# Performance work log

Hardware: AMD Instinct MI355X
Metric: run time of the kernel (lower is better)

The kernel has to match this reference:

```python
import jax, jax.numpy as jnp
import numpy as np
from jax import lax

SLOPE = 0.01  # nn.LeakyReLU default negative slope

def leaky(x):
    return jnp.where(x >= 0, x, SLOPE * x)

def conv2d(x, w, b, pad):
    # x: [N,C,H,W], w: [O,I,kh,kw]
    y = lax.conv_general_dilated(x, w, (1, 1), [(pad, pad), (pad, pad)],
                                 dimension_numbers=('NCHW', 'OIHW', 'NCHW'))
    return y + b[None, :, None, None]

def centered_ifftn(x, axes):
    # np.fft.fftshift(np.fft.ifftn(np.fft.ifftshift(X), norm='ortho'))
    return jnp.fft.fftshift(jnp.fft.ifftn(jnp.fft.ifftshift(x, axes=axes), axes=axes, norm='ortho'), axes=axes)

def setup_inputs() -> dict:
    key = jax.random.key(0)
    ks = jax.random.split(key, 10)
    B, H, W, CK = 8, 640, 368, 32
    return {
        'img':    jax.random.normal(ks[0], (B, 1, H, W), jnp.float32),
        'kspace': jax.random.normal(ks[1], (B, 2, H, W), jnp.float32),
        # k_model1: Conv2d(2, CK, 3, padding=1) + LeakyReLU
        'wk': jax.random.normal(ks[2], (CK, 2, 3, 3), jnp.float32) * 0.1,
        'bk': jnp.zeros((CK,), jnp.float32),
        # conv1: Conv2d(CK, 2, kernel_size=1)
        'w1': jax.random.normal(ks[3], (2, CK, 1, 1), jnp.float32) * 0.1,
        'b1': jnp.zeros((2,), jnp.float32),
        # conv2: Conv2d(2, 1, kernel_size=1)
        'w2': jax.random.normal(ks[4], (1, 2, 1, 1), jnp.float32) * 0.1,
        'b2': jnp.zeros((1,), jnp.float32),
        # i_model1: Conv2d(1, 1, 3, padding=1) + LeakyReLU
        'wi': jax.random.normal(ks[5], (1, 1, 3, 3), jnp.float32) * 0.1,
        'bi': jnp.zeros((1,), jnp.float32),
    }

def reference(img, kspace, wk, bk, w1, b1, w2, b2, wi, bi):
    # k-space branch: k_model1 then conv1 + LeakyReLU
    out1 = leaky(conv2d(leaky(conv2d(kspace, wk, bk, 1)), w1, b1, 0))  # [B,2,H,W]
    # channel 0 = real, channel 1 = imag; ifftn over ALL axes (incl. batch),
    # exactly as the original numpy call with axes=range(out.ndim)
    cplx = out1[:, 0].astype(jnp.complex64) + 1j * out1[:, 1].astype(jnp.complex64)  # [B,H,W]
    im = jnp.abs(centered_ifftn(cplx, (0, 1, 2)))[:, None]  # [B,1,H,W]
    # concat with image, cast to half (torch.cuda.HalfTensor), conv2 + LeakyReLU
    out = jnp.concatenate([im, img], axis=1).astype(jnp.float16)  # [B,2,H,W]
    out = leaky(conv2d(out, w2.astype(jnp.float16), b2.astype(jnp.float16), 0))
    out = out.astype(jnp.float32)  # [B,1,H,W]
    # image-domain model
    return leaky(conv2d(out, wi, bi, 1))  # [B,1,H,W]
```

## Files before the change

### kernel.cpp

```cpp
#include <hip/hip_runtime.h>
#include <hip/hip_fp16.h>
#include <math.h>

#define B_ 8
#define H_ 640
#define W_ 368
#define HW_ (H_*W_)
#define NP_ (B_*H_*W_)

#define WLINES 8
#define HCOLS 4
#define TS 16

typedef __attribute__((ext_vector_type(8))) short v8s;
typedef __attribute__((ext_vector_type(4))) float v4f;

__device__ __forceinline__ float leaky_(float x){ return x >= 0.f ? x : 0.01f*x; }

__device__ __forceinline__ unsigned short f2bf(float x){
    unsigned u = __float_as_uint(x);
    u += 0x7FFFu + ((u >> 16) & 1u);
    return (unsigned short)(u >> 16);
}

__device__ __forceinline__ float2 cadd_(float2 a, float2 b){ return make_float2(a.x+b.x, a.y+b.y); }
__device__ __forceinline__ float2 csub_(float2 a, float2 b){ return make_float2(a.x-b.x, a.y-b.y); }
__device__ __forceinline__ float2 cmul_(float2 a, float c, float s){
    return make_float2(a.x*c - a.y*s, a.x*s + a.y*c);
}
__device__ __forceinline__ float2 cmulv_(float2 a, float2 w){
    return make_float2(a.x*w.x - a.y*w.y, a.x*w.y + a.y*w.x);
}

__device__ __forceinline__ void dft4p_(float2 p0, float2 p1, float2 p2, float2 p3,
                                       float2& z0, float2& z1, float2& z2, float2& z3){
    float2 s0 = cadd_(p0,p2), d0 = csub_(p0,p2);
    float2 s1 = cadd_(p1,p3), d1 = csub_(p1,p3);
    z0 = cadd_(s0,s1);
    z2 = csub_(s0,s1);
    z1 = make_float2(d0.x - d1.y, d0.y + d1.x);
    z3 = make_float2(d0.x + d1.y, d0.y - d1.x);
}

__device__ __forceinline__ void fft16p_(const float2* x, float2* X){
    const float C1 = 0.9238795325112867f, S1 = 0.3826834323650898f;
    const float R  = 0.7071067811865476f;
    float2 Y[4][4];
    #pragma unroll
    for (int b = 0; b < 4; ++b)
        dft4p_(x[b], x[4+b], x[8+b], x[12+b], Y[b][0], Y[b][1], Y[b][2], Y[b][3]);
    Y[1][1] = cmul_(Y[1][1],  C1,  S1);
    Y[1][2] = cmul_(Y[1][2],   R,   R);
    Y[1][3] = cmul_(Y[1][3],  S1,  C1);
    Y[2][1] = cmul_(Y[2][1],   R,   R);
    Y[2][2] = make_float2(-Y[2][2].y, Y[2][2].x);
    Y[2][3] = cmul_(Y[2][3],  -R,   R);
    Y[3][1] = cmul_(Y[3][1],  S1,  C1);
    Y[3][2] = cmul_(Y[3][2],  -R,   R);
    Y[3][3] = cmul_(Y[3][3], -C1, -S1);
    #pragma unroll
    for (int c = 0; c < 4; ++c)
        dft4p_(Y[0][c], Y[1][c], Y[2][c], Y[3][c], X[c], X[c+4], X[c+8], X[c+12]);
}

__device__ __forceinline__ void fft8p_(const float2* x, float2* X){
    const float R = 0.7071067811865476f;
    float2 Y0[4], Y1[4];
    dft4p_(x[0], x[2], x[4], x[6], Y0[0], Y0[1], Y0[2], Y0[3]);
    dft4p_(x[1], x[3], x[5], x[7], Y1[0], Y1[1], Y1[2], Y1[3]);
    float2 T0 = Y1[0];
    float2 T1 = cmul_(Y1[1],  R, R);
    float2 T2 = make_float2(-Y1[2].y, Y1[2].x);
    float2 T3 = cmul_(Y1[3], -R, R);
    X[0] = cadd_(Y0[0], T0);  X[4] = csub_(Y0[0], T0);
    X[1] = cadd_(Y0[1], T1);  X[5] = csub_(Y0[1], T1);
    X[2] = cadd_(Y0[2], T2);  X[6] = csub_(Y0[2], T2);
    X[3] = cadd_(Y0[3], T3);  X[7] = csub_(Y0[3], T3);
}

__global__ void init_tables_kernel(float2* __restrict__ T){
    int i = blockIdx.x*blockDim.x + threadIdx.x;
    if (i >= 1301) return;
    int r, c, modN; int j;
    if      (i <  368){ j = i;        r = j%16; c = j/16; modN = 368; }
    else if (i < 1008){ j = i-368;    r = j%16; c = j/16; modN = 640; }
    else if (i < 1048){ j = i-1008;   r = j%8;  c = j/8;  modN = 40;  }
    else              { j = i-1048;   r = j/11; c = j%11 + 1; modN = 23; }
    int t = (int)(((long long)r * c) % modN);
    if (t > modN/2) t -= modN;
    float ang = (float)(6.283185307179586 * ((double)t / (double)modN));
    float s, co;
    sincosf(ang, &s, &co);
    T[i] = make_float2(co, s);
}

__global__ __launch_bounds__(256) void kbranch_mfma(const float* __restrict__ ksp,
                               const float* __restrict__ wk,
                               const float* __restrict__ bk,
                               const float* __restrict__ w1,
                               const float* __restrict__ b1,
                               float2* __restrict__ A){
    __shared__ unsigned short Sb[2616];
    __shared__ unsigned short Wr[4*512];
    int t = threadIdx.x;
    int bh = blockIdx.x;
    int h = bh % 640, b = bh / 640;

    for (int i = t; i < 2616; i += 256){
        float val = 0.f;
        if (i < 2232){
            int rr = i / 372, col = i - rr*372;
            int r = rr >> 1, ic = rr & 1;
            int hh = h - 1 + r, sc = col - 1;
            if ((unsigned)hh < 640u && (unsigned)sc < 368u)
                val = ksp[((b*2 + ic)*640 + hh)*368 + sc];
        }
        Sb[i] = f2bf(val);
    }

    int lane = t & 63, wave = t >> 6;
    int oc = lane & 15, q = lane >> 4;
    int off[8];
    v8s bf0, bf1, b2f;
    #pragma unroll
    for (int j = 0; j < 8; ++j){
        int kk = q*8 + j;
        if (kk < 18){
            int ic = (kk >= 9) ? 1 : 0;
            int tt = kk - ic*9;
            int ty = tt/3, tx = tt - ty*3;
            off[j] = (ty*2 + ic)*372 + tx;
            bf0[j] = (short)f2bf(wk[oc*18 + kk]);
            bf1[j] = (short)f2bf(wk[(oc+16)*18 + kk]);
        } else {
            off[j] = 2232;
            bf0[j] = 0; bf1[j] = 0;
        }
        b2f[j] = (oc < 2) ? (short)f2bf(w1[oc*32 + kk]) : (short)0;
    }
    float bk0 = bk[oc], bk1 = bk[oc+16];
    float biasn = (oc == 1) ? b1[1] : b1[0];
    unsigned short* Wrw = Wr + (wave << 9);
    __syncthreads();

    int gbase = wave*6;
    int cnt = (wave < 3) ? 6 : 5;
    for (int i = 0; i < cnt; ++i){
        int g = gbase + i;
        int w0m = g*16 + oc;
        v8s af;
        #pragma unroll
        for (int j = 0; j < 8; ++j) af[j] = (short)Sb[off[j] + w0m];
        v4f d0 = {0.f,0.f,0.f,0.f}, d1 = {0.f,0.f,0.f,0.f};
        d0 = __builtin_amdgcn_mfma_f32_16x16x32_bf16(af, bf0, d0, 0, 0, 0);
        d1 = __builtin_amdgcn_mfma_f32_16x16x32_bf16(af, bf1, d1, 0, 0, 0);
        #pragma unroll
        for (int r = 0; r < 4; ++r){
            int px = q*4 + r;
            Wrw[px*32 + oc]      = f2bf(leaky_(d0[r] + bk0));
            Wrw[px*32 + 16 + oc] = f2bf(leaky_(d1[r] + bk1));
        }
        asm volatile("s_waitcnt lgkmcnt(0)" ::: "memory");
        const v8s* ap = (const v8s*)(Wrw + oc*32);
        v8s a2 = ap[q];
        v4f d2 = {0.f,0.f,0.f,0.f};
        d2 = __builtin_amdgcn_mfma_f32_16x16x32_bf16(a2, b2f, d2, 0, 0, 0);
        float vals[4], ov[4];
        #pragma unroll
        for (int r = 0; r < 4; ++r){
            vals[r] = leaky_(biasn + d2[r]);
            ov[r] = __shfl_xor(vals[r], 1);
        }
        if (oc == 0){
            float2* dst = A + (size_t)bh*368 + g*16 + q*4;
            *(float4*)dst       = make_float4(vals[0], ov[0], vals[1], ov[1]);
            *(float4*)(dst + 2) = make_float4(vals[2], ov[2], vals[3], ov[3]);
        }
        asm volatile("s_waitcnt lgkmcnt(0)" ::: "memory");
    }
}

__global__ __launch_bounds__(256) void fftW_kernel(const float2* __restrict__ A,
                                                   const float2* __restrict__ TW368P,
                                                   const float2* __restrict__ F23P,
                                                   float2* __restrict__ Bo){
    __shared__ float2 X[WLINES*369];
    int t = threadIdx.x;
    size_t base = (size_t)blockIdx.x * (WLINES*368);

    for (int i = t; i < WLINES*368; i += 256){
        int l = i / 368, n = i - l*368;
        float2 v = A[base + i];
        float s = (i & 1) ? -1.f : 1.f;
        X[l*369 + n] = make_float2(v.x*s, v.y*s);
    }
    __syncthreads();

    if (t < 184){
        int l = t & 7, n2 = t >> 3;
        float2 xr[16], Xo[16];
        #pragma unroll
        for (int n1 = 0; n1 < 16; ++n1) xr[n1] = X[l*369 + 23*n1 + n2];
        fft16p_(xr, Xo);
        const float2* row = TW368P + n2*16;
        #pragma unroll
        for (int k1 = 0; k1 < 16; ++k1)
            X[l*369 + 23*k1 + n2] = cmulv_(Xo[k1], row[k1]);
    }
    __syncthreads();

    {
        int l = t & 7, k1 = (t >> 3) & 15, half = t >> 7;
        const float2* xp = X + l*369 + 23*k1;
        float2 x0 = xp[0];
        float2 u[11], d[11];
        #pragma unroll
        for (int m = 1; m <= 11; ++m){
            float2 a = xp[m], bb = xp[23-m];
            u[m-1] = cadd_(a, bb);
            d[m-1] = csub_(a, bb);
        }
        __syncthreads();
        int k2beg = half ? 12 : 0;
        int k2end = half ? 23 : 12;
        for (int k2 = k2beg; k2 < k2end; ++k2){
            const float2* row = F23P + k2*11;
            float re = x0.x, im = x0.y;
            #pragma unroll
            for (int m = 0; m < 11; ++m){
                float c = row[m].x, s = row[m].y;
                re += u[m].x*c - d[m].y*s;
                im += u[m].y*c + d[m].x*s;
            }
            X[l*369 + k1 + 16*k2] = make_float2(re, im);
        }
    }
    __syncthreads();

    const float sc = 0.052129458158616354f;
    for (int i = t; i < WLINES*368; i += 256){
        int l = i / 368, k = i - l*368;
        float2 v = X[l*369 + k];
        float s = (i & 1) ? -sc : sc;
        Bo[base + i] = make_float2(v.x*s, v.y*s);
    }
}

__global__ __launch_bounds__(256) void fftH_kernel(const float2* __restrict__ Bi,
                                                   const float2* __restrict__ TW640P,
                                                   const float2* __restrict__ TW40P,
                                                   float2* __restrict__ Ao){
    __shared__ float2 X[640*5];
    int t = threadIdx.x;
    int b  = blockIdx.x / 92;
    int w0 = (blockIdx.x - b*92) * HCOLS;
    const float2* src = Bi + (size_t)b*HW_ + w0;

    for (int i = t; i < 640*HCOLS; i += 256){
        int n = i >> 2, c = i & 3;
        float2 v = src[(size_t)n*W_ + c];
        float s = (n & 1) ? -1.f : 1.f;
        X[n*5 + c] = make_float2(v.x*s, v.y*s);
    }
    __syncthreads();

    if (t < 160){
        int c = t & 3, n2 = t >> 2;
        float2 xr[16], Xo[16];
        #pragma unroll
        for (int n1 = 0; n1 < 16; ++n1) xr[n1] = X[(40*n1 + n2)*5 + c];
        fft16p_(xr, Xo);
        const float2* row = TW640P + n2*16;
        #pragma unroll
        for (int k1 = 0; k1 < 16; ++k1)
            X[(40*k1 + n2)*5 + c] = cmulv_(Xo[k1], row[k1]);
    }
    __syncthreads();

    for (int it = t; it < 320; it += 256){
        int c = it & 3, k1 = (it >> 2) & 15, m2 = it >> 6;
        float2 xr[8], Xo[8];
        #pragma unroll
        for (int m1 = 0; m1 < 8; ++m1) xr[m1] = X[(40*k1 + 5*m1 + m2)*5 + c];
        fft8p_(xr, Xo);
        const float2* row = TW40P + m2*8;
        #pragma unroll
        for (int j1 = 0; j1 < 8; ++j1)
            X[(40*k1 + 5*j1 + m2)*5 + c] = cmulv_(Xo[j1], row[j1]);
    }
    __syncthreads();

    {
        const float CK1[5] = {1.f,  0.30901699437494745f, -0.8090169943749475f, -0.8090169943749475f,  0.30901699437494745f};
        const float SK1[5] = {0.f,  0.9510565162951535f,   0.5877852522924731f, -0.5877852522924731f, -0.9510565162951535f};
        const float CK2[5] = {1.f, -0.8090169943749475f,   0.30901699437494745f, 0.30901699437494745f, -0.8090169943749475f};
        const float SK2[5] = {0.f,  0.5877852522924731f,  -0.9510565162951535f,  0.9510565162951535f, -0.5877852522924731f};
        int it0 = t, it1 = t + 256;
        int c0 = it0 & 3, k10 = (it0 >> 2) & 15, j10 = it0 >> 6;
        int c1 = it1 & 3, k11 = (it1 >> 2) & 15, j11 = it1 >> 6;
        float2 p0[5], p1[5];
        #pragma unroll
        for (int m2 = 0; m2 < 5; ++m2) p0[m2] = X[(40*k10 + 5*j10 + m2)*5 + c0];
        #pragma unroll
        for (int m2 = 0; m2 < 5; ++m2) p1[m2] = X[(40*k11 + 5*j11 + m2)*5 + c1];
        __syncthreads();
        float2 u0a = cadd_(p0[1], p0[4]), d0a = csub_(p0[1], p0[4]);
        float2 u0b = cadd_(p0[2], p0[3]), d0b = csub_(p0[2], p0[3]);
        float2 u1a = cadd_(p1[1], p1[4]), d1a = csub_(p1[1], p1[4]);
        float2 u1b = cadd_(p1[2], p1[3]), d1b = csub_(p1[2], p1[3]);
        #pragma unroll
        for (int j2 = 0; j2 < 5; ++j2){
            float c1v = CK1[j2], s1v = SK1[j2], c2v = CK2[j2], s2v = SK2[j2];
            float re0 = p0[0].x + u0a.x*c1v - d0a.y*s1v + u0b.x*c2v - d0b.y*s2v;
            float im0 = p0[0].y + u0a.y*c1v + d0a.x*s1v + u0b.y*c2v + d0b.x*s2v;
            float re1 = p1[0].x + u1a.x*c1v - d1a.y*s1v + u1b.x*c2v - d1b.y*s2v;
            float im1 = p1[0].y + u1a.y*c1v + d1a.x*s1v + u1b.y*c2v + d1b.x*s2v;
            X[(k10 + 16*j10 + 128*j2)*5 + c0] = make_float2(re0, im0);
            X[(k11 + 16*j11 + 128*j2)*5 + c1] = make_float2(re1, im1);
        }
    }
    __syncthreads();

    const float sc = 0.03952847075210474f;
    float2* dst = Ao + (size_t)b*HW_ + w0;
    for (int i = t; i < 640*HCOLS; i += 256){
        int k = i >> 2, c = i & 3;
        float2 v = X[k*5 + c];
        float s = (k & 1) ? -sc : sc;
        dst[(size_t)k*W_ + c] = make_float2(v.x*s, v.y*s);
    }
}

__global__ __launch_bounds__(256) void tail_kernel(const float2* __restrict__ A,
                                  const float* __restrict__ img,
                                  const float* __restrict__ w2,
                                  const float* __restrict__ b2,
                                  const float* __restrict__ wi,
                                  const float* __restrict__ bi,
                                  float* __restrict__ out){
    __shared__ float Pl[8][TS+2][TS+2];
    int t = threadIdx.x;
    int ty0 = (blockIdx.x / 23) * TS;
    int tx0 = (blockIdx.x % 23) * TS;

    float w2h0 = __half2float(__float2half(w2[0]));
    float w2h1 = __half2float(__float2half(w2[1]));
    float b2h  = __half2float(__float2half(b2[0]));
    const float sc8 = 0.35355339059327373f;

    for (int idx = t; idx < (TS+2)*(TS+2); idx += 256){
        int hy = idx / (TS+2), hx = idx - hy*(TS+2);
        int hh = ty0 - 1 + hy, ww = tx0 - 1 + hx;
        bool inb = (hh >= 0) && (hh < H_) && (ww >= 0) && (ww < W_);
        int hc = min(max(hh, 0), H_-1), wc = min(max(ww, 0), W_-1);
        int hw = hc*W_ + wc;
        float2 x[8], Xo[8];
        #pragma unroll
        for (int n = 0; n < 8; ++n){
            float2 v = A[(size_t)n*HW_ + hw];
            float s = (n & 1) ? -1.f : 1.f;
            x[n] = make_float2(v.x*s, v.y*s);
        }
        fft8p_(x, Xo);
        float inbf = inb ? 1.f : 0.f;
        #pragma unroll
        for (int k = 0; k < 8; ++k){
            float s = (k & 1) ? -sc8 : sc8;
            float yr = Xo[k].x * s, yi = Xo[k].y * s;
            float mag = sqrtf(yr*yr + yi*yi);
            float a = __half2float(__float2half(mag));
            float g = __half2float(__float2half(img[(size_t)k*HW_ + hw]));
            float o = a*w2h0 + g*w2h1 + b2h;
            o = leaky_(o);
            o = __half2float(__float2half(o));
            Pl[k][hy][hx] = o * inbf;
        }
    }
    __syncthreads();

    int sy = t >> 4, sx = t & 15;
    float wv[9];
    #pragma unroll
    for (int q = 0; q < 9; ++q) wv[q] = wi[q];
    float bi0 = bi[0];
    #pragma unroll
    for (int k = 0; k < 8; ++k){
        float acc = bi0;
        #pragma unroll
        for (int dy = 0; dy < 3; ++dy)
            #pragma unroll
            for (int dx = 0; dx < 3; ++dx)
                acc += wv[dy*3+dx] * Pl[k][sy+dy][sx+dx];
        out[((size_t)k*H_ + ty0+sy)*W_ + tx0+sx] = leaky_(acc);
    }
}

extern "C" void kernel_launch(void* const* d_in, const int* in_sizes, int n_in,
                              void* d_out, int out_size, void* d_ws, size_t ws_size,
                              hipStream_t stream){
    const float* img = (const float*)d_in[0];
    const float* ksp = (const float*)d_in[1];
    const float* wk  = (const float*)d_in[2];
    const float* bk  = (const float*)d_in[3];
    const float* w1  = (const float*)d_in[4];
    const float* b1  = (const float*)d_in[5];
    const float* w2  = (const float*)d_in[6];
    const float* b2  = (const float*)d_in[7];
    const float* wi  = (const float*)d_in[8];
    const float* bi  = (const float*)d_in[9];

    char* ws = (char*)d_ws;
    float2* A   = (float2*)(ws + 0);
    float2* Bb  = (float2*)(ws + 15073280);
    float2* T   = (float2*)(ws + 30146560);
    float2* TW368P = T + 0;
    float2* TW640P = T + 368;
    float2* TW40P  = T + 1008;
    float2* F23P   = T + 1048;
    float* out  = (float*)d_out;

    init_tables_kernel<<<6, 256, 0, stream>>>(T);

    kbranch_mfma<<<B_*H_, 256, 0, stream>>>(ksp, wk, bk, w1, b1, A);

    fftW_kernel<<<(B_*H_)/WLINES, 256, 0, stream>>>(A, TW368P, F23P, Bb);
    fftH_kernel<<<B_*(W_/HCOLS), 256, 0, stream>>>(Bb, TW640P, TW40P, A);

    tail_kernel<<<(H_/TS)*(W_/TS), 256, 0, stream>>>(A, img, w2, b2, wi, bi, out);
}
```

Measured before the change: 172.6 us.

## Stage im2col patches in LDS for vectorized MFMA A-fragment loads

The k-branch conv kernel now builds a per-row im2col matrix in shared memory (368 pixels × 40 padded taps) instead of a raw halo tile. Each MFMA A-fragment becomes one 16-byte LDS load rather than eight scattered 2-byte loads. The intermediate 32-channel activations are written back into the same buffer as packed pairs, with the w1 weight order permuted to match, and one waitcnt and the separate Wr buffer are dropped. Leaky ReLU becomes fmaxf. The risks are a slower staging phase (strided stores, 144 active threads issuing scalar global loads) and possible races from reusing M across waves.

New measurement: 173.5 us. Within noise of the previous version (+0.5%).

```diff
diff --git a/kernel.cpp b/kernel.cpp
--- a/kernel.cpp
+++ b/kernel.cpp
@@ -15,7 +15,7 @@
 typedef __attribute__((ext_vector_type(8))) short v8s;
 typedef __attribute__((ext_vector_type(4))) float v4f;
 
-__device__ __forceinline__ float leaky_(float x){ return x >= 0.f ? x : 0.01f*x; }
+__device__ __forceinline__ float leaky_(float x){ return fmaxf(x, 0.01f*x); }
 
 __device__ __forceinline__ unsigned short f2bf(float x){
     unsigned u = __float_as_uint(x);
@@ -100,69 +100,69 @@
                                const float* __restrict__ w1,
                                const float* __restrict__ b1,
                                float2* __restrict__ A){
-    __shared__ unsigned short Sb[2616];
-    __shared__ unsigned short Wr[4*512];
+    __shared__ unsigned short M[368*40];
     int t = threadIdx.x;
     int bh = blockIdx.x;
     int h = bh % 640, b = bh / 640;
-
-    for (int i = t; i < 2616; i += 256){
-        float val = 0.f;
-        if (i < 2232){
-            int rr = i / 372, col = i - rr*372;
-            int r = rr >> 1, ic = rr & 1;
-            int hh = h - 1 + r, sc = col - 1;
-            if ((unsigned)hh < 640u && (unsigned)sc < 368u)
-                val = ksp[((b*2 + ic)*640 + hh)*368 + sc];
-        }
-        Sb[i] = f2bf(val);
-    }
-
     int lane = t & 63, wave = t >> 6;
-    int oc = lane & 15, q = lane >> 4;
-    int off[8];
+    int n = lane & 15, q = lane >> 4;
+
     v8s bf0, bf1, b2f;
     #pragma unroll
     for (int j = 0; j < 8; ++j){
         int kk = q*8 + j;
-        if (kk < 18){
-            int ic = (kk >= 9) ? 1 : 0;
-            int tt = kk - ic*9;
-            int ty = tt/3, tx = tt - ty*3;
-            off[j] = (ty*2 + ic)*372 + tx;
-            bf0[j] = (short)f2bf(wk[oc*18 + kk]);
-            bf1[j] = (short)f2bf(wk[(oc+16)*18 + kk]);
-        } else {
-            off[j] = 2232;
-            bf0[j] = 0; bf1[j] = 0;
-        }
-        b2f[j] = (oc < 2) ? (short)f2bf(w1[oc*32 + kk]) : (short)0;
-    }
-    float bk0 = bk[oc], bk1 = bk[oc+16];
-    float biasn = (oc == 1) ? b1[1] : b1[0];
-    unsigned short* Wrw = Wr + (wave << 9);
+        float v0 = (kk < 18) ? wk[n*18 + kk]      : 0.f;
+        float v1 = (kk < 18) ? wk[(n+16)*18 + kk] : 0.f;
+        bf0[j] = (short)f2bf(v0);
+        bf1[j] = (short)f2bf(v1);
+        int ko = (kk & 1) ? 16 + (kk >> 1) : (kk >> 1);
+        b2f[j] = (n < 2) ? (short)f2bf(w1[n*32 + ko]) : (short)0;
+    }
+    float bk0 = bk[n], bk1 = bk[n+16];
+    float biasn = (n == 1) ? b1[1] : b1[0];
+
+    if (t < 144){
+        int kk = t >> 3, px0 = t & 7;
+        int ic = (kk >= 9) ? 1 : 0;
+        int tt = kk - 9*ic;
+        int ty = tt / 3, tx = tt - 3*ty;
+        int hh = h - 1 + ty;
+        float rvf = ((unsigned)hh < 640u) ? 1.f : 0.f;
+        int hhc = min(max(hh, 0), 639);
+        const float* base = ksp + ((size_t)(b*2 + ic)*640 + hhc)*368;
+        int txo = tx - 1;
+        for (int px = px0; px < 368; px += 8){
+            int c = px + txo;
+            float msk = ((unsigned)c < 368u) ? rvf : 0.f;
+            int cc = min(max(c, 0), 367);
+            M[px*40 + kk] = f2bf(base[cc] * msk);
+        }
+    } else {
+        int kk = 18 + ((t - 144) >> 3), px0 = (t - 144) & 7;
+        for (int px = px0; px < 368; px += 8)
+            M[px*40 + kk] = 0;
+    }
     __syncthreads();
 
     int gbase = wave*6;
     int cnt = (wave < 3) ? 6 : 5;
     for (int i = 0; i < cnt; ++i){
         int g = gbase + i;
-        int w0m = g*16 + oc;
-        v8s af;
-        #pragma unroll
-        for (int j = 0; j < 8; ++j) af[j] = (short)Sb[off[j] + w0m];
+        int pxa = g*16 + n;
+        const v8s af = *(const v8s*)(M + pxa*40 + q*8);
         v4f d0 = {0.f,0.f,0.f,0.f}, d1 = {0.f,0.f,0.f,0.f};
         d0 = __builtin_amdgcn_mfma_f32_16x16x32_bf16(af, bf0, d0, 0, 0, 0);
         d1 = __builtin_amdgcn_mfma_f32_16x16x32_bf16(af, bf1, d1, 0, 0, 0);
         #pragma unroll
         for (int r = 0; r < 4; ++r){
-            int px = q*4 + r;
-            Wrw[px*32 + oc]      = f2bf(leaky_(d0[r] + bk0));
-            Wrw[px*32 + 16 + oc] = f2bf(leaky_(d1[r] + bk1));
+            int px = g*16 + q*4 + r;
+            float l0 = leaky_(d0[r] + bk0);
+            float l1 = leaky_(d1[r] + bk1);
+            unsigned pk = ((unsigned)f2bf(l1) << 16) | (unsigned)f2bf(l0);
+            *(unsigned*)(M + px*40 + 2*n) = pk;
         }
         asm volatile("s_waitcnt lgkmcnt(0)" ::: "memory");
-        const v8s* ap = (const v8s*)(Wrw + oc*32);
-        v8s a2 = ap[q];
+        const v8s a2 = *(const v8s*)(M + pxa*40 + q*8);
         v4f d2 = {0.f,0.f,0.f,0.f};
         d2 = __builtin_amdgcn_mfma_f32_16x16x32_bf16(a2, b2f, d2, 0, 0, 0);
         float vals[4], ov[4];
@@ -171,12 +171,11 @@
             vals[r] = leaky_(biasn + d2[r]);
             ov[r] = __shfl_xor(vals[r], 1);
         }
-        if (oc == 0){
+        if (n == 0){
             float2* dst = A + (size_t)bh*368 + g*16 + q*4;
             *(float4*)dst       = make_float4(vals[0], ov[0], vals[1], ov[1]);
             *(float4*)(dst + 2) = make_float4(vals[2], ov[2], vals[3], ov[3]);
         }
-        asm volatile("s_waitcnt lgkmcnt(0)" ::: "memory");
     }
 }
 
```

## Transpose intermediate after W-FFT so H-FFT reads contiguous columns

Applied to the files above, without the earlier changes.

The W-direction FFT now writes its output transposed ([b][w][h]), so the H-direction FFT kernel loads contiguous 640-element lines instead of strided 4-column gathers. It uses a padded per-line shared layout in place of the interleaved one. The tail kernel now reads the transposed layout and iterates its halo with h as the fast index to keep reads coalesced, which splits its work into two LDS passes. The change trades coalescing on the W-FFT store (8 consecutive h values per k) for contiguous H-FFT loads and stores, and it also makes leaky_ branchless via fmaxf.

Result: no change. 172.8 us (+0.1%).

```diff
diff --git a/kernel.cpp b/kernel.cpp
--- a/kernel.cpp
+++ b/kernel.cpp
@@ -9,13 +9,14 @@
 #define NP_ (B_*H_*W_)
 
 #define WLINES 8
-#define HCOLS 4
+#define HLINES 4
+#define HP 645
 #define TS 16
 
 typedef __attribute__((ext_vector_type(8))) short v8s;
 typedef __attribute__((ext_vector_type(4))) float v4f;
 
-__device__ __forceinline__ float leaky_(float x){ return x >= 0.f ? x : 0.01f*x; }
+__device__ __forceinline__ float leaky_(float x){ return fmaxf(x, 0.01f*x); }
 
 __device__ __forceinline__ unsigned short f2bf(float x){
     unsigned u = __float_as_uint(x);
@@ -183,7 +184,7 @@
 __global__ __launch_bounds__(256) void fftW_kernel(const float2* __restrict__ A,
                                                    const float2* __restrict__ TW368P,
                                                    const float2* __restrict__ F23P,
-                                                   float2* __restrict__ Bo){
+                                                   float2* __restrict__ Bt){
     __shared__ float2 X[WLINES*369];
     int t = threadIdx.x;
     size_t base = (size_t)blockIdx.x * (WLINES*368);
@@ -191,7 +192,7 @@
     for (int i = t; i < WLINES*368; i += 256){
         int l = i / 368, n = i - l*368;
         float2 v = A[base + i];
-        float s = (i & 1) ? -1.f : 1.f;
+        float s = (n & 1) ? -1.f : 1.f;
         X[l*369 + n] = make_float2(v.x*s, v.y*s);
     }
     __syncthreads();
@@ -238,55 +239,55 @@
     __syncthreads();
 
     const float sc = 0.052129458158616354f;
+    int b  = blockIdx.x / 80;
+    int h0 = (blockIdx.x - b*80) * WLINES;
     for (int i = t; i < WLINES*368; i += 256){
-        int l = i / 368, k = i - l*368;
+        int k = i >> 3, l = i & 7;
         float2 v = X[l*369 + k];
-        float s = (i & 1) ? -sc : sc;
-        Bo[base + i] = make_float2(v.x*s, v.y*s);
-    }
-}
-
-__global__ __launch_bounds__(256) void fftH_kernel(const float2* __restrict__ Bi,
+        float s = (k & 1) ? -sc : sc;
+        Bt[((size_t)(b*368 + k))*640 + h0 + l] = make_float2(v.x*s, v.y*s);
+    }
+}
+
+__global__ __launch_bounds__(256) void fftH_kernel(const float2* __restrict__ Bt,
                                                    const float2* __restrict__ TW640P,
                                                    const float2* __restrict__ TW40P,
-                                                   float2* __restrict__ Ao){
-    __shared__ float2 X[640*5];
+                                                   float2* __restrict__ A2){
+    __shared__ float2 X[HLINES*HP];
     int t = threadIdx.x;
-    int b  = blockIdx.x / 92;
-    int w0 = (blockIdx.x - b*92) * HCOLS;
-    const float2* src = Bi + (size_t)b*HW_ + w0;
-
-    for (int i = t; i < 640*HCOLS; i += 256){
-        int n = i >> 2, c = i & 3;
-        float2 v = src[(size_t)n*W_ + c];
+    size_t base = (size_t)blockIdx.x * (HLINES*640);
+
+    for (int i = t; i < HLINES*640; i += 256){
+        int l = i / 640, n = i - l*640;
+        float2 v = Bt[base + i];
         float s = (n & 1) ? -1.f : 1.f;
-        X[n*5 + c] = make_float2(v.x*s, v.y*s);
+        X[l*HP + n] = make_float2(v.x*s, v.y*s);
     }
     __syncthreads();
 
     if (t < 160){
-        int c = t & 3, n2 = t >> 2;
+        int l = t & 3, n2 = t >> 2;
         float2 xr[16], Xo[16];
         #pragma unroll
-        for (int n1 = 0; n1 < 16; ++n1) xr[n1] = X[(40*n1 + n2)*5 + c];
+        for (int n1 = 0; n1 < 16; ++n1) xr[n1] = X[l*HP + 40*n1 + n2];
         fft16p_(xr, Xo);
         const float2* row = TW640P + n2*16;
         #pragma unroll
         for (int k1 = 0; k1 < 16; ++k1)
-            X[(40*k1 + n2)*5 + c] = cmulv_(Xo[k1], row[k1]);
+            X[l*HP + 40*k1 + n2] = cmulv_(Xo[k1], row[k1]);
     }
     __syncthreads();
 
     for (int it = t; it < 320; it += 256){
-        int c = it & 3, k1 = (it >> 2) & 15, m2 = it >> 6;
+        int l = it & 3, k1 = (it >> 2) & 15, m2 = it >> 6;
         float2 xr[8], Xo[8];
         #pragma unroll
-        for (int m1 = 0; m1 < 8; ++m1) xr[m1] = X[(40*k1 + 5*m1 + m2)*5 + c];
+        for (int m1 = 0; m1 < 8; ++m1) xr[m1] = X[l*HP + 40*k1 + 5*m1 + m2];
         fft8p_(xr, Xo);
         const float2* row = TW40P + m2*8;
         #pragma unroll
         for (int j1 = 0; j1 < 8; ++j1)
-            X[(40*k1 + 5*j1 + m2)*5 + c] = cmulv_(Xo[j1], row[j1]);
+            X[l*HP + 40*k1 + 5*j1 + m2] = cmulv_(Xo[j1], row[j1]);
     }
     __syncthreads();
 
@@ -296,13 +297,13 @@
         const float CK2[5] = {1.f, -0.8090169943749475f,   0.30901699437494745f, 0.30901699437494745f, -0.8090169943749475f};
         const float SK2[5] = {0.f,  0.5877852522924731f,  -0.9510565162951535f,  0.9510565162951535f, -0.5877852522924731f};
         int it0 = t, it1 = t + 256;
-        int c0 = it0 & 3, k10 = (it0 >> 2) & 15, j10 = it0 >> 6;
-        int c1 = it1 & 3, k11 = (it1 >> 2) & 15, j11 = it1 >> 6;
+        int l0 = it0 & 3, k10 = (it0 >> 2) & 15, j10 = it0 >> 6;
+        int l1 = it1 & 3, k11 = (it1 >> 2) & 15, j11 = it1 >> 6;
         float2 p0[5], p1[5];
         #pragma unroll
-        for (int m2 = 0; m2 < 5; ++m2) p0[m2] = X[(40*k10 + 5*j10 + m2)*5 + c0];
-        #pragma unroll
-        for (int m2 = 0; m2 < 5; ++m2) p1[m2] = X[(40*k11 + 5*j11 + m2)*5 + c1];
+        for (int m2 = 0; m2 < 5; ++m2) p0[m2] = X[l0*HP + 40*k10 + 5*j10 + m2];
+        #pragma unroll
+        for (int m2 = 0; m2 < 5; ++m2) p1[m2] = X[l1*HP + 40*k11 + 5*j11 + m2];
         __syncthreads();
         float2 u0a = cadd_(p0[1], p0[4]), d0a = csub_(p0[1], p0[4]);
         float2 u0b = cadd_(p0[2], p0[3]), d0b = csub_(p0[2], p0[3]);
@@ -315,30 +316,29 @@
             float im0 = p0[0].y + u0a.y*c1v + d0a.x*s1v + u0b.y*c2v + d0b.x*s2v;
             float re1 = p1[0].x + u1a.x*c1v - d1a.y*s1v + u1b.x*c2v - d1b.y*s2v;
             float im1 = p1[0].y + u1a.y*c1v + d1a.x*s1v + u1b.y*c2v + d1b.x*s2v;
-            X[(k10 + 16*j10 + 128*j2)*5 + c0] = make_float2(re0, im0);
-            X[(k11 + 16*j11 + 128*j2)*5 + c1] = make_float2(re1, im1);
+            X[l0*HP + k10 + 16*j10 + 128*j2] = make_float2(re0, im0);
+            X[l1*HP + k11 + 16*j11 + 128*j2] = make_float2(re1, im1);
         }
     }
     __syncthreads();
 
     const float sc = 0.03952847075210474f;
-    float2* dst = Ao + (size_t)b*HW_ + w0;
-    for (int i = t; i < 640*HCOLS; i += 256){
-        int k = i >> 2, c = i & 3;
-        float2 v = X[k*5 + c];
+    for (int i = t; i < HLINES*640; i += 256){
+        int l = i / 640, k = i - l*640;
+        float2 v = X[l*HP + k];
         float s = (k & 1) ? -sc : sc;
-        dst[(size_t)k*W_ + c] = make_float2(v.x*s, v.y*s);
-    }
-}
-
-__global__ __launch_bounds__(256) void tail_kernel(const float2* __restrict__ A,
+        A2[base + i] = make_float2(v.x*s, v.y*s);
+    }
+}
+
+__global__ __launch_bounds__(256) void tail_kernel(const float2* __restrict__ A2,
                                   const float* __restrict__ img,
                                   const float* __restrict__ w2,
                                   const float* __restrict__ b2,
                                   const float* __restrict__ wi,
                                   const float* __restrict__ bi,
                                   float* __restrict__ out){
-    __shared__ float Pl[8][TS+2][TS+2];
+    __shared__ float Pl[8][TS+2][TS+3];
     int t = threadIdx.x;
     int ty0 = (blockIdx.x / 23) * TS;
     int tx0 = (blockIdx.x % 23) * TS;
@@ -347,31 +347,40 @@
     float w2h1 = __half2float(__float2half(w2[1]));
     float b2h  = __half2float(__float2half(b2[0]));
     const float sc8 = 0.35355339059327373f;
+
+    for (int idx = t; idx < (TS+2)*(TS+2); idx += 256){
+        int hx = idx / (TS+2), hy = idx - hx*(TS+2);
+        int hh = ty0 - 1 + hy, ww = tx0 - 1 + hx;
+        int hc = min(max(hh, 0), H_-1), wc = min(max(ww, 0), W_-1);
+        float2 x[8], Xo[8];
+        #pragma unroll
+        for (int n = 0; n < 8; ++n){
+            float2 v = A2[((size_t)(n*368 + wc))*640 + hc];
+            float s = (n & 1) ? -1.f : 1.f;
+            x[n] = make_float2(v.x*s, v.y*s);
+        }
+        fft8p_(x, Xo);
+        #pragma unroll
+        for (int k = 0; k < 8; ++k){
+            float s = (k & 1) ? -sc8 : sc8;
+            float yr = Xo[k].x * s, yi = Xo[k].y * s;
+            float mag = sqrtf(yr*yr + yi*yi);
+            Pl[k][hy][hx] = __half2float(__float2half(mag));
+        }
+    }
+    __syncthreads();
 
     for (int idx = t; idx < (TS+2)*(TS+2); idx += 256){
         int hy = idx / (TS+2), hx = idx - hy*(TS+2);
         int hh = ty0 - 1 + hy, ww = tx0 - 1 + hx;
         bool inb = (hh >= 0) && (hh < H_) && (ww >= 0) && (ww < W_);
         int hc = min(max(hh, 0), H_-1), wc = min(max(ww, 0), W_-1);
-        int hw = hc*W_ + wc;
-        float2 x[8], Xo[8];
-        #pragma unroll
-        for (int n = 0; n < 8; ++n){
-            float2 v = A[(size_t)n*HW_ + hw];
-            float s = (n & 1) ? -1.f : 1.f;
-            x[n] = make_float2(v.x*s, v.y*s);
-        }
-        fft8p_(x, Xo);
         float inbf = inb ? 1.f : 0.f;
         #pragma unroll
         for (int k = 0; k < 8; ++k){
-            float s = (k & 1) ? -sc8 : sc8;
-            float yr = Xo[k].x * s, yi = Xo[k].y * s;
-            float mag = sqrtf(yr*yr + yi*yi);
-            float a = __half2float(__float2half(mag));
-            float g = __half2float(__float2half(img[(size_t)k*HW_ + hw]));
-            float o = a*w2h0 + g*w2h1 + b2h;
-            o = leaky_(o);
+            float g = __half2float(__float2half(img[(size_t)k*HW_ + hc*W_ + wc]));
+            float a = Pl[k][hy][hx];
+            float o = leaky_(a*w2h0 + g*w2h1 + b2h);
             o = __half2float(__float2half(o));
             Pl[k][hy][hx] = o * inbf;
         }
@@ -411,7 +420,7 @@
 
     char* ws = (char*)d_ws;
     float2* A   = (float2*)(ws + 0);
-    float2* Bb  = (float2*)(ws + 15073280);
+    float2* Bt  = (float2*)(ws + 15073280);
     float2* T   = (float2*)(ws + 30146560);
     float2* TW368P = T + 0;
     float2* TW640P = T + 368;
@@ -423,8 +432,8 @@
 
     kbranch_mfma<<<B_*H_, 256, 0, stream>>>(ksp, wk, bk, w1, b1, A);
 
-    fftW_kernel<<<(B_*H_)/WLINES, 256, 0, stream>>>(A, TW368P, F23P, Bb);
-    fftH_kernel<<<B_*(W_/HCOLS), 256, 0, stream>>>(Bb, TW640P, TW40P, A);
+    fftW_kernel<<<(B_*H_)/WLINES, 256, 0, stream>>>(A, TW368P, F23P, Bt);
+    fftH_kernel<<<(B_*W_)/HLINES, 256, 0, stream>>>(Bt, TW640P, TW40P, A);
 
     tail_kernel<<<(H_/TS)*(W_/TS), 256, 0, stream>>>(A, img, w2, b2, wi, bi, out);
 }
```
